# Kernel tuning notes

Hardware: AMD Instinct MI355X
Metric: run time of the kernel (lower is better)

## Reference

```python
import jax, jax.numpy as jnp
import numpy as np

B, L, NF, H = 4, 1024, 480, 32
FC = NF + H          # feat_i_classes = 512
D = FC               # downsample_feats (default None -> feat_i_classes)
W = 65               # positional window width (odd -> 'same' padding matches)
MAX0, MAX1 = 10.0, 100.0  # max_std_sigma_0 / max_std_sigma_1


def _uni(k, shape, lo=-0.01, hi=0.01):
    return jax.random.uniform(k, shape, jnp.float32, lo, hi)


def setup_inputs() -> dict:
    key = jax.random.key(0)
    ks = jax.random.split(key, 11)
    return {
        "x_embeds": jax.random.normal(ks[0], (B, L, NF), jnp.float32),
        "latent_outputs": jax.random.normal(ks[1], (B, L, H), jnp.float32),
        "masks": jnp.ones((B, L, 1), jnp.float32),
        "pos_embed": (jnp.arange(W, dtype=jnp.float32) - W // 2).reshape(W, 1, 1),
        "x": jax.random.uniform(ks[2], (B, L, 23), jnp.float32),
        "all_x_all_ampl": _uni(ks[3], (5, D, H)),
        "inp_decomp_vecs": _uni(ks[4], (5, D, 1)),
        "out_decomp_vecs": _uni(ks[5], (5, 1, H)),
        "all_x_all_bias": _uni(ks[6], (5, 1, H)),
        "pos_dep_ampl_weights": _uni(ks[7], (1, FC, H)),
        "knn_activations": _uni(ks[8], (2, FC, D)),
    }


def _conv_same(x_bdl, w_hdw):
    # torch F.conv1d (cross-correlation), stride 1, padding 'same'
    return jax.lax.conv_general_dilated(
        x_bdl, w_hdw, window_strides=(1,), padding="SAME",
        dimension_numbers=("NCH", "OIH", "NCH"))


def reference(x_embeds, latent_outputs, masks, pos_embed, x,
              all_x_all_ampl, inp_decomp_vecs, out_decomp_vecs,
              all_x_all_bias, pos_dep_ampl_weights, knn_activations):
    A = all_x_all_ampl                       # (5,D,H)
    rec = lambda i: inp_decomp_vecs[i] * out_decomp_vecs[i]  # (D,1)*(1,H)->(D,H)
    inv_c0 = 1.0 / MAX0 ** 2

    cls = jax.nn.softmax(latent_outputs * masks, axis=-1) * masks
    oef = jnp.concatenate([x_embeds, cls], axis=-1)          # (B,L,FC)
    cf0 = oef @ knn_activations[0]                           # (B,L,D)
    cf1 = oef @ knn_activations[1]                           # (B,L,D)

    def kern(ampl, mean, inv_var):
        # cos(0*pos+0)=1; pos (W,1,1) broadcast vs (D,H) -> (W,D,H)
        return jnp.exp(-inv_var * (pos_embed - mean) ** 2) * ampl

    # torch: std=abs(w)**0.5; inv_var = std**2 + 1/max0**2 = abs(w)+c
    k0 = kern(A[0], rec(0), jnp.abs(rec(1)) + inv_c0)
    k1 = kern(A[1], 0.0,    jnp.abs(rec(2)) + inv_c0)
    k2 = kern(A[2], rec(3), jnp.abs(rec(4)) + inv_c0)

    conv = lambda f, k: _conv_same(f.transpose(0, 2, 1),
                                   k.transpose(2, 1, 0)).transpose(0, 2, 1)
    acts0 = conv(cf0, k0)                                    # (B,L,H)
    acts1 = conv(cf1, k1)
    acts2 = conv(cf0, k2)

    b0, b1, b2, b3, class_mult = all_x_all_bias              # each (1,H)
    rec_dist_filt = (acts0 + b0) * acts1 \
        + acts2 * (cf1 @ A[1] + b2) \
        + (cf0 @ A[3] + b1) * (cf1 @ A[4])

    collect = jnp.sum(x[..., 21:], axis=-1, keepdims=True)   # (B,L,1)
    m = (masks + collect)[..., 0]                            # (B,L)
    pos = jnp.arange(L, dtype=jnp.float32)
    rel2 = (pos[None, :] - pos[:, None]) ** 2                # (L,L)
    sig = class_mult[0] ** 2 + 1.0 / MAX1 ** 2               # (H,)
    G = jnp.exp(-sig[:, None, None] * rel2)                  # (H,L,L)
    # V_correction[b,i,h] = m[b,i] * sum_j G[h,i,j] m[b,j]  (mask is rank-1)
    Vc = m[:, :, None] * jnp.einsum("hij,bj->bih", G, m)     # (B,L,H)

    per_pos = oef @ pos_dep_ampl_weights[0] + b3             # (B,L,H)
    return Vc * per_pos * rec_dist_filt * masks
```

## Files before the change

kernel.cpp:

```cpp
#include <hip/hip_runtime.h>
#include <hip/hip_bf16.h>

#define BB 4
#define LL 1024
#define NFE 480
#define HH 32
#define FCC 512
#define DD 512
#define WW 65
#define BL (BB*LL)
#define BLH (BL*HH)
#define LPAD 1088

typedef short bf16x8 __attribute__((ext_vector_type(8)));
typedef float f32x16 __attribute__((ext_vector_type(16)));
typedef unsigned short us8 __attribute__((ext_vector_type(8)));

__device__ inline unsigned short f2bf(float x) {
    union { float f; unsigned u; } v; v.f = x;
    unsigned r = v.u + 0x7FFFu + ((v.u >> 16) & 1u);
    return (unsigned short)(r >> 16);
}

__device__ __align__(16) unsigned short g_oefb[BL*FCC];
__device__ __align__(16) unsigned short g_knt[2*DD*FCC];
__device__ float  g_m[BL];
__device__ __align__(16) unsigned short g_fpad[2*BB*LPAD*DD];
__device__ __align__(16) unsigned short g_kb2[(size_t)3*WW*4*8*64*8];
__device__ __align__(16) unsigned short g_kbs[4*4*8*64*8];
__device__ float  g_actsp[4][3*BLH];
__device__ float  g_small[4*BLH];
__device__ float  g_gt[HH*LL];
__device__ float  g_vsum4[4][BLH];

__global__ __launch_bounds__(256) void kprep(const float* __restrict__ x_embeds,
                                             const float* __restrict__ latent,
                                             const float* __restrict__ masks,
                                             const float* __restrict__ x,
                                             const float* __restrict__ ampl,
                                             const float* __restrict__ inp,
                                             const float* __restrict__ outv,
                                             const float* __restrict__ pos,
                                             const float* __restrict__ bias,
                                             const float* __restrict__ pdw,
                                             const float* __restrict__ knn) {
    const int bx = blockIdx.x;
    const int tid = threadIdx.x;

    if (bx < 512) {
        const int row0 = bx * 8;
        const int r    = row0 + (tid >> 5);
        const int lane = tid & 31;

        const float mask = masks[r];
        float v = latent[r*HH + lane] * mask;
        float mx = v;
        #pragma unroll
        for (int off = 16; off > 0; off >>= 1) mx = fmaxf(mx, __shfl_xor(mx, off, 32));
        float e = __expf(v - mx);
        float s = e;
        #pragma unroll
        for (int off = 16; off > 0; off >>= 1) s += __shfl_xor(s, off, 32);
        g_oefb[r*FCC + NFE + lane] = f2bf(e / s * mask);

        if (lane == 0) g_m[r] = mask + x[r*23 + 21] + x[r*23 + 22];

        for (int idx = tid; idx < 8*NFE; idx += 256) {
            int rr = idx / NFE, c = idx - rr*NFE;
            g_oefb[(row0+rr)*FCC + c] = f2bf(x_embeds[(row0+rr)*NFE + c]);
        }
    } else if (bx < 640) {
        int idx = (bx - 512) * 256 + tid;
        int fzb = idx >> 12;
        int rem = idx & 4095;
        int rowi = rem >> 6;
        int col8 = rem & 63;
        int row = (rowi < 32) ? rowi : (1024 + rowi);
        int4 z = make_int4(0,0,0,0);
        *reinterpret_cast<int4*>(&g_fpad[((size_t)fzb*LPAD + row)*DD + col8*8]) = z;
    } else if (bx < 768) {
        __shared__ unsigned short tile[64][65];
        int idx2 = bx - 640;
        const int k0 = (idx2 & 7) * 64;
        const int n0 = ((idx2 >> 3) & 7) * 64;
        const int z  = idx2 >> 6;
        const float* __restrict__ src = knn + (size_t)z*FCC*DD;
        #pragma unroll 4
        for (int i = 0; i < 16; ++i) {
            int idx = i*256 + tid;
            int kk = idx >> 6, nn = idx & 63;
            tile[kk][nn] = f2bf(src[(size_t)(k0+kk)*DD + n0+nn]);
        }
        __syncthreads();
        #pragma unroll 4
        for (int i = 0; i < 16; ++i) {
            int idx = i*256 + tid;
            int nn = idx >> 6, kk = idx & 63;
            g_knt[((size_t)z*DD + n0+nn)*FCC + k0+kk] = tile[kk][nn];
        }
    } else if (bx < 800) {
        int t = (bx - 768)*256 + tid;
        int lane = t & 63;
        int ks = (t >> 6) & 7;
        int dt = (t >> 9) & 3;
        int o  = t >> 11;
        int l31 = lane & 31, khalf = lane >> 5;
        const float* S = (o == 0) ? ampl + 1*DD*HH :
                         (o == 1) ? ampl + 3*DD*HH :
                         (o == 2) ? ampl + 4*DD*HH : pdw;
        int k0 = dt*128 + ks*16 + khalf*8;
        us8 outw;
        #pragma unroll
        for (int i = 0; i < 8; ++i) outw[i] = f2bf(S[(size_t)(k0+i)*HH + l31]);
        *reinterpret_cast<us8*>(&g_kbs[(size_t)t*8]) = outw;
    } else if (bx < 928) {
        int idx = (bx - 800) * 256 + tid;
        int h = idx & 31;
        int dist = idx >> 5;
        float cm = bias[4*HH + h];
        float sig = cm*cm + 1e-4f;
        float dd = (float)dist;
        g_gt[idx] = __expf(-sig * dd * dd);
    } else {
        int idx3 = bx - 928;
        int xi  = idx3 & 7;
        int rem = idx3 >> 3;
        int w   = rem % 65;
        int z   = rem / 65;
        int idx = xi * 256 + tid;
        const int lane = idx & 63;
        const int ks   = (idx >> 6) & 7;
        const int dt   = idx >> 9;
        const int h    = lane & 31;
        const int d8   = dt*128 + ks*16 + (lane >> 5)*8;

        const float c0 = 0.01f;
        const float p = pos[w];
        int ai, mi, vi;
        if (z == 0)      { ai = 0; mi = 0;  vi = 1; }
        else if (z == 1) { ai = 1; mi = -1; vi = 2; }
        else             { ai = 2; mi = 3;  vi = 4; }

        us8 outw;
        #pragma unroll
        for (int i = 0; i < 8; ++i) {
            int d = d8 + i;
            float a    = ampl[(size_t)ai*DD*HH + d*HH + h];
            float mean = (mi >= 0) ? inp[mi*DD + d] * outv[mi*HH + h] : 0.f;
            float iv   = fabsf(inp[vi*DD + d] * outv[vi*HH + h]) + c0;
            float tt = p - mean;
            outw[i] = f2bf(__expf(-iv * tt * tt) * a);
        }
        *reinterpret_cast<us8*>(&g_kb2[((((size_t)z*WW + w)*4 + dt)*8 + ks)*512 + (size_t)lane*8]) = outw;
    }
}

__global__ __launch_bounds__(256) void k2_mfma() {
    const int nt = blockIdx.x;
    const int mt = blockIdx.y;
    const int z  = blockIdx.z;
    const int t  = threadIdx.x;
    const int wave = t >> 6, lane = t & 63;
    const int l31 = lane & 31, khalf = lane >> 5;
    const int n0 = nt*128 + wave*32;
    const int m_base = mt*64;

    __shared__ __align__(16) unsigned short smem[64*128];

    f32x16 acc[2];
    #pragma unroll
    for (int mti = 0; mti < 2; ++mti)
        #pragma unroll
        for (int i = 0; i < 16; ++i) acc[mti][i] = 0.f;

    const unsigned short* __restrict__ bptr =
        g_knt + ((size_t)z*DD + n0 + l31)*FCC + khalf*8;

    for (int kc = 0; kc < 4; ++kc) {
        __syncthreads();
        const unsigned short* __restrict__ src = g_oefb + (size_t)m_base*FCC + kc*128;
        #pragma unroll
        for (int c = 0; c < 4; ++c) {
            int q = c*256 + t;
            int row = q >> 4, slot = q & 15;
            int4 v = *reinterpret_cast<const int4*>(src + (size_t)row*FCC + slot*8);
            int off = row*256 + ((slot*16) ^ ((row & 15) << 4));
            *reinterpret_cast<int4*>((char*)smem + off) = v;
        }
        __syncthreads();
        #pragma unroll
        for (int ks = 0; ks < 8; ++ks) {
            bf16x8 bf = *reinterpret_cast<const bf16x8*>(bptr + kc*128 + ks*16);
            int dby = ks*32 + khalf*16;
            #pragma unroll
            for (int mti = 0; mti < 2; ++mti) {
                int r = mti*32 + l31;
                bf16x8 a = *reinterpret_cast<const bf16x8*>(
                    (char*)smem + r*256 + (dby ^ ((r & 15) << 4)));
                acc[mti] = __builtin_amdgcn_mfma_f32_32x32x16_bf16(a, bf, acc[mti], 0, 0, 0);
            }
        }
    }

    #pragma unroll
    for (int mti = 0; mti < 2; ++mti) {
        #pragma unroll
        for (int reg = 0; reg < 16; ++reg) {
            int rowf = (reg & 3) + 8*(reg >> 2) + 4*khalf;
            int m = m_base + mti*32 + rowf;
            int b_ = m >> 10, l_ = m & 1023;
            g_fpad[((size_t)(z*BB + b_)*LPAD + 32 + l_)*DD + n0 + l31] = f2bf(acc[mti][reg]);
        }
    }
}

__global__ __launch_bounds__(256) void kheavy() {
    __shared__ __align__(16) char smem_raw[32768];
    const int bx = blockIdx.x;
    const int t  = threadIdx.x;

    if (bx < 768) {
        const int xcd = bx & 7;
        const int j8  = bx >> 3;
        const int gidx = xcd*96 + j8;
        const int zdq = gidx >> 6;
        const int g   = gidx & 63;
        const int lt = g & 15;
        const int b  = g >> 4;
        const int z  = zdq >> 2;
        const int dq = zdq & 3;
        const int fz = (z == 1) ? 1 : 0;
        const int wave = t >> 6, lane = t & 63;
        const int l31 = lane & 31, khalf = lane >> 5;

        const int wbeg = (wave == 0) ? 0 : 17 + (wave - 1)*16;
        const int wend = (wave == 0) ? 17 : wbeg + 16;

        f32x16 acc0, acc1;
        #pragma unroll
        for (int i = 0; i < 16; ++i) { acc0[i] = 0.f; acc1[i] = 0.f; }

        const unsigned short* src =
            g_fpad + ((size_t)(fz*BB + b)*LPAD + lt*64) * DD + dq*128;
        #pragma unroll
        for (int c = 0; c < 8; ++c) {
            int q = c*256 + t;
            int row = q >> 4, slot = q & 15;
            int4 v = *reinterpret_cast<const int4*>(src + (size_t)row*DD + slot*8);
            int off = row*256 + ((slot*16) ^ ((row & 15) << 4));
            *reinterpret_cast<int4*>(smem_raw + off) = v;
        }
        __syncthreads();

        for (int w = wbeg; w < wend; ++w) {
            const unsigned short* kbw =
                g_kb2 + ((((size_t)z*WW + w)*4 + dq)*8)*512;
            const int r0 = l31 + w;
            const int r1 = r0 + 32;
            #pragma unroll
            for (int ks = 0; ks < 8; ++ks) {
                bf16x8 bf = *reinterpret_cast<const bf16x8*>(kbw + ks*512 + lane*8);
                int dby = ks*32 + khalf*16;
                bf16x8 a0 = *reinterpret_cast<const bf16x8*>(
                    smem_raw + r0*256 + (dby ^ ((r0 & 15) << 4)));
                bf16x8 a1 = *reinterpret_cast<const bf16x8*>(
                    smem_raw + r1*256 + (dby ^ ((r1 & 15) << 4)));
                acc0 = __builtin_amdgcn_mfma_f32_32x32x16_bf16(a0, bf, acc0, 0, 0, 0);
                acc1 = __builtin_amdgcn_mfma_f32_32x32x16_bf16(a1, bf, acc1, 0, 0, 0);
            }
        }

        __syncthreads();
        float* red = (float*)smem_raw;
        #pragma unroll
        for (int reg = 0; reg < 16; ++reg) {
            int row = (reg & 3) + 8*(reg >> 2) + 4*khalf;
            red[wave*2048 + row*32 + l31]        = acc0[reg];
            red[wave*2048 + (32 + row)*32 + l31] = acc1[reg];
        }
        __syncthreads();
        float* outp = g_actsp[dq] + (size_t)z*BLH + ((size_t)b*LL + lt*64)*HH;
        #pragma unroll
        for (int j = 0; j < 8; ++j) {
            int i = j*256 + t;
            float sum = red[i] + red[2048 + i] + red[4096 + i] + red[6144 + i];
            outp[i] = sum;
        }
    } else if (bx < 1280) {
        float* mlT = (float*)smem_raw;
        const int g  = bx - 768;
        const int jq = g >> 7;
        const int ib = g & 127;
        const int i0 = ib * 8;

        int wlo = i0 - 352; if (wlo < 0) wlo = 0; else wlo &= ~3;
        int whi = i0 + 360; if (whi > 1024) whi = 1024; else whi = (whi + 3) & ~3;
        int qstep = (((whi - wlo) + 15) >> 4) << 2;
        int qlo = wlo + jq*qstep;
        int qhi = qlo + qstep; if (qhi > whi) qhi = whi;
        int qn = qhi - qlo; if (qn < 0) qn = 0;

        for (int idx = t; idx < qn*4; idx += 256) {
            int jj = idx >> 2, b = idx & 3;
            mlT[jj*4 + b] = g_m[b*LL + qlo + jj];
        }
        __syncthreads();

        const int h = t & 31;
        const int i = i0 + (t >> 5);
        const float* __restrict__ gtt = g_gt;
        float a0 = 0.f, a1 = 0.f, a2 = 0.f, a3 = 0.f;
        #pragma unroll 2
        for (int jj = 0; jj < qn; ++jj) {
            int j = qlo + jj;
            int c = i - j; int d = c < 0 ? -c : c;
            float gv = gtt[d*HH + h];
            float4 mv = *reinterpret_cast<const float4*>(&mlT[jj*4]);
            a0 = fmaf(gv, mv.x, a0);
            a1 = fmaf(gv, mv.y, a1);
            a2 = fmaf(gv, mv.z, a2);
            a3 = fmaf(gv, mv.w, a3);
        }
        float* vs = g_vsum4[jq];
        vs[(size_t)(0*LL + i)*HH + h]      = a0;
        vs[(size_t)(1*LL + i)*HH + h + BLH/4*0 + 1*LL*HH*0] = a1;
        vs[((size_t)(1*LL + i))*HH + h] = a1;
        vs[((size_t)(2*LL + i))*HH + h] = a2;
        vs[((size_t)(3*LL + i))*HH + h] = a3;
    } else {
        const int g = bx - 1280;
        const int mt = g & 31;
        const int o  = g >> 5;
        const int wave = t >> 6, lane = t & 63;
        const int l31 = lane & 31, khalf = lane >> 5;

        const unsigned short* src;
        if (o == 3) {
            src = g_oefb + (size_t)mt*128*FCC;
        } else {
            const int fz = (o == 1) ? 0 : 1;
            const int m0 = mt*128;
            const int b_ = m0 >> 10, l0 = m0 & 1023;
            src = g_fpad + ((size_t)(fz*BB + b_)*LPAD + 32 + l0)*DD;
        }

        f32x16 acc;
        #pragma unroll
        for (int i = 0; i < 16; ++i) acc[i] = 0.f;

        for (int kc = 0; kc < 4; ++kc) {
            __syncthreads();
            const unsigned short* s2 = src + kc*128;
            #pragma unroll
            for (int c = 0; c < 8; ++c) {
                int q = c*256 + t;
                int row = q >> 4, slot = q & 15;
                int4 v = *reinterpret_cast<const int4*>(s2 + (size_t)row*512 + slot*8);
                int off = row*256 + ((slot*16) ^ ((row & 15) << 4));
                *reinterpret_cast<int4*>(smem_raw + off) = v;
            }
            __syncthreads();
            #pragma unroll
            for (int ks = 0; ks < 8; ++ks) {
                bf16x8 bf = *reinterpret_cast<const bf16x8*>(
                    &g_kbs[((((size_t)o*4 + kc)*8 + ks)*64 + lane)*8]);
                int dby = ks*32 + khalf*16;
                int r = wave*32 + l31;
                bf16x8 a = *reinterpret_cast<const bf16x8*>(
                    smem_raw + r*256 + (dby ^ ((r & 15) << 4)));
                acc = __builtin_amdgcn_mfma_f32_32x32x16_bf16(a, bf, acc, 0, 0, 0);
            }
        }

        float* outp = g_small + (size_t)o*BLH + ((size_t)mt*128 + wave*32)*HH;
        #pragma unroll
        for (int reg = 0; reg < 16; ++reg) {
            int row = (reg & 3) + 8*(reg >> 2) + 4*khalf;
            outp[(size_t)row*HH + l31] = acc[reg];
        }
    }
}

__global__ __launch_bounds__(256) void k7_final(const float* __restrict__ masks,
                                                const float* __restrict__ bias,
                                                float* __restrict__ out) {
    int idx = blockIdx.x * 256 + threadIdx.x;
    int r = idx >> 5, h = idx & 31;
    float a0 = 0.f, a1 = 0.f, a2 = 0.f;
    #pragma unroll
    for (int s = 0; s < 4; ++s) {
        a0 += g_actsp[s][idx];
        a1 += g_actsp[s][BLH + idx];
        a2 += g_actsp[s][2*BLH + idx];
    }
    float rdf = (a0 + bias[0*HH + h]) * a1
              + a2 * (g_small[idx] + bias[2*HH + h])
              + (g_small[BLH + idx] + bias[1*HH + h]) * g_small[2*BLH + idx];
    float pp = g_small[3*BLH + idx] + bias[3*HH + h];
    float vc = g_m[r] * (g_vsum4[0][idx] + g_vsum4[1][idx] + g_vsum4[2][idx] + g_vsum4[3][idx]);
    out[idx] = vc * pp * rdf * masks[r];
}

extern "C" void kernel_launch(void* const* d_in, const int* in_sizes, int n_in,
                              void* d_out, int out_size, void* d_ws, size_t ws_size,
                              hipStream_t stream) {
    (void)in_sizes; (void)n_in; (void)d_ws; (void)ws_size; (void)out_size;
    const float* x_embeds = (const float*)d_in[0];
    const float* latent   = (const float*)d_in[1];
    const float* masks    = (const float*)d_in[2];
    const float* pos      = (const float*)d_in[3];
    const float* x        = (const float*)d_in[4];
    const float* ampl     = (const float*)d_in[5];
    const float* inp      = (const float*)d_in[6];
    const float* outv     = (const float*)d_in[7];
    const float* bias     = (const float*)d_in[8];
    const float* pdw      = (const float*)d_in[9];
    const float* knn      = (const float*)d_in[10];
    float* out = (float*)d_out;

    hipLaunchKernelGGL(kprep, dim3(2488), dim3(256), 0, stream,
                       x_embeds, latent, masks, x, ampl, inp, outv, pos, bias, pdw, knn);
    hipLaunchKernelGGL(k2_mfma, dim3(4, 64, 2), dim3(256), 0, stream);
    hipLaunchKernelGGL(kheavy, dim3(1408), dim3(256), 0, stream);
    hipLaunchKernelGGL(k7_final, dim3(BLH/256), dim3(256), 0, stream, masks, bias, out);
}
```

Baseline: 77.53 us.

## Move Gaussian vsum into GEMM kernel and split conv window across twice the blocks

```diff
diff --git a/kernel.cpp b/kernel.cpp
--- a/kernel.cpp
+++ b/kernel.cpp
@@ -28,7 +28,7 @@
 __device__ __align__(16) unsigned short g_fpad[2*BB*LPAD*DD];
 __device__ __align__(16) unsigned short g_kb2[(size_t)3*WW*4*8*64*8];
 __device__ __align__(16) unsigned short g_kbs[4*4*8*64*8];
-__device__ float  g_actsp[4][3*BLH];
+__device__ float  g_actsp[8][3*BLH];
 __device__ float  g_small[4*BLH];
 __device__ float  g_gt[HH*LL];
 __device__ float  g_vsum4[4][BLH];
@@ -155,140 +155,69 @@
     }
 }
 
-__global__ __launch_bounds__(256) void k2_mfma() {
-    const int nt = blockIdx.x;
-    const int mt = blockIdx.y;
-    const int z  = blockIdx.z;
-    const int t  = threadIdx.x;
-    const int wave = t >> 6, lane = t & 63;
-    const int l31 = lane & 31, khalf = lane >> 5;
-    const int n0 = nt*128 + wave*32;
-    const int m_base = mt*64;
-
-    __shared__ __align__(16) unsigned short smem[64*128];
-
-    f32x16 acc[2];
-    #pragma unroll
-    for (int mti = 0; mti < 2; ++mti)
-        #pragma unroll
-        for (int i = 0; i < 16; ++i) acc[mti][i] = 0.f;
-
-    const unsigned short* __restrict__ bptr =
-        g_knt + ((size_t)z*DD + n0 + l31)*FCC + khalf*8;
-
-    for (int kc = 0; kc < 4; ++kc) {
-        __syncthreads();
-        const unsigned short* __restrict__ src = g_oefb + (size_t)m_base*FCC + kc*128;
-        #pragma unroll
-        for (int c = 0; c < 4; ++c) {
-            int q = c*256 + t;
-            int row = q >> 4, slot = q & 15;
-            int4 v = *reinterpret_cast<const int4*>(src + (size_t)row*FCC + slot*8);
-            int off = row*256 + ((slot*16) ^ ((row & 15) << 4));
-            *reinterpret_cast<int4*>((char*)smem + off) = v;
-        }
-        __syncthreads();
-        #pragma unroll
-        for (int ks = 0; ks < 8; ++ks) {
-            bf16x8 bf = *reinterpret_cast<const bf16x8*>(bptr + kc*128 + ks*16);
-            int dby = ks*32 + khalf*16;
-            #pragma unroll
-            for (int mti = 0; mti < 2; ++mti) {
-                int r = mti*32 + l31;
-                bf16x8 a = *reinterpret_cast<const bf16x8*>(
-                    (char*)smem + r*256 + (dby ^ ((r & 15) << 4)));
-                acc[mti] = __builtin_amdgcn_mfma_f32_32x32x16_bf16(a, bf, acc[mti], 0, 0, 0);
-            }
-        }
-    }
-
-    #pragma unroll
-    for (int mti = 0; mti < 2; ++mti) {
-        #pragma unroll
-        for (int reg = 0; reg < 16; ++reg) {
-            int rowf = (reg & 3) + 8*(reg >> 2) + 4*khalf;
-            int m = m_base + mti*32 + rowf;
-            int b_ = m >> 10, l_ = m & 1023;
-            g_fpad[((size_t)(z*BB + b_)*LPAD + 32 + l_)*DD + n0 + l31] = f2bf(acc[mti][reg]);
-        }
-    }
-}
-
-__global__ __launch_bounds__(256) void kheavy() {
-    __shared__ __align__(16) char smem_raw[32768];
+__global__ __launch_bounds__(256) void k2k6() {
+    __shared__ __align__(16) char smem_raw[16384];
     const int bx = blockIdx.x;
     const int t  = threadIdx.x;
 
-    if (bx < 768) {
-        const int xcd = bx & 7;
-        const int j8  = bx >> 3;
-        const int gidx = xcd*96 + j8;
-        const int zdq = gidx >> 6;
-        const int g   = gidx & 63;
-        const int lt = g & 15;
-        const int b  = g >> 4;
-        const int z  = zdq >> 2;
-        const int dq = zdq & 3;
-        const int fz = (z == 1) ? 1 : 0;
+    if (bx < 512) {
+        const int nt = bx & 3;
+        const int mt = (bx >> 2) & 63;
+        const int z  = bx >> 8;
         const int wave = t >> 6, lane = t & 63;
         const int l31 = lane & 31, khalf = lane >> 5;
-
-        const int wbeg = (wave == 0) ? 0 : 17 + (wave - 1)*16;
-        const int wend = (wave == 0) ? 17 : wbeg + 16;
-
-        f32x16 acc0, acc1;
-        #pragma unroll
-        for (int i = 0; i < 16; ++i) { acc0[i] = 0.f; acc1[i] = 0.f; }
-
-        const unsigned short* src =
-            g_fpad + ((size_t)(fz*BB + b)*LPAD + lt*64) * DD + dq*128;
-        #pragma unroll
-        for (int c = 0; c < 8; ++c) {
-            int q = c*256 + t;
-            int row = q >> 4, slot = q & 15;
-            int4 v = *reinterpret_cast<const int4*>(src + (size_t)row*DD + slot*8);
-            int off = row*256 + ((slot*16) ^ ((row & 15) << 4));
-            *reinterpret_cast<int4*>(smem_raw + off) = v;
-        }
-        __syncthreads();
-
-        for (int w = wbeg; w < wend; ++w) {
-            const unsigned short* kbw =
-                g_kb2 + ((((size_t)z*WW + w)*4 + dq)*8)*512;
-            const int r0 = l31 + w;
-            const int r1 = r0 + 32;
+        const int n0 = nt*128 + wave*32;
+        const int m_base = mt*64;
+        unsigned short* smem = (unsigned short*)smem_raw;
+
+        f32x16 acc[2];
+        #pragma unroll
+        for (int mti = 0; mti < 2; ++mti)
+            #pragma unroll
+            for (int i = 0; i < 16; ++i) acc[mti][i] = 0.f;
+
+        const unsigned short* __restrict__ bptr =
+            g_knt + ((size_t)z*DD + n0 + l31)*FCC + khalf*8;
+
+        for (int kc = 0; kc < 4; ++kc) {
+            __syncthreads();
+            const unsigned short* __restrict__ src = g_oefb + (size_t)m_base*FCC + kc*128;
+            #pragma unroll
+            for (int c = 0; c < 4; ++c) {
+                int q = c*256 + t;
+                int row = q >> 4, slot = q & 15;
+                int4 v = *reinterpret_cast<const int4*>(src + (size_t)row*FCC + slot*8);
+                int off = row*256 + ((slot*16) ^ ((row & 15) << 4));
+                *reinterpret_cast<int4*>(smem_raw + off) = v;
+            }
+            __syncthreads();
             #pragma unroll
             for (int ks = 0; ks < 8; ++ks) {
-                bf16x8 bf = *reinterpret_cast<const bf16x8*>(kbw + ks*512 + lane*8);
+                bf16x8 bf = *reinterpret_cast<const bf16x8*>(bptr + kc*128 + ks*16);
                 int dby = ks*32 + khalf*16;
-                bf16x8 a0 = *reinterpret_cast<const bf16x8*>(
-                    smem_raw + r0*256 + (dby ^ ((r0 & 15) << 4)));
-                bf16x8 a1 = *reinterpret_cast<const bf16x8*>(
-                    smem_raw + r1*256 + (dby ^ ((r1 & 15) << 4)));
-                acc0 = __builtin_amdgcn_mfma_f32_32x32x16_bf16(a0, bf, acc0, 0, 0, 0);
-                acc1 = __builtin_amdgcn_mfma_f32_32x32x16_bf16(a1, bf, acc1, 0, 0, 0);
-            }
-        }
-
-        __syncthreads();
-        float* red = (float*)smem_raw;
-        #pragma unroll
-        for (int reg = 0; reg < 16; ++reg) {
-            int row = (reg & 3) + 8*(reg >> 2) + 4*khalf;
-            red[wave*2048 + row*32 + l31]        = acc0[reg];
-            red[wave*2048 + (32 + row)*32 + l31] = acc1[reg];
-        }
-        __syncthreads();
-        float* outp = g_actsp[dq] + (size_t)z*BLH + ((size_t)b*LL + lt*64)*HH;
-        #pragma unroll
-        for (int j = 0; j < 8; ++j) {
-            int i = j*256 + t;
-            float sum = red[i] + red[2048 + i] + red[4096 + i] + red[6144 + i];
-            outp[i] = sum;
-        }
-    } else if (bx < 1280) {
+                #pragma unroll
+                for (int mti = 0; mti < 2; ++mti) {
+                    int r = mti*32 + l31;
+                    bf16x8 a = *reinterpret_cast<const bf16x8*>(
+                        smem_raw + r*256 + (dby ^ ((r & 15) << 4)));
+                    acc[mti] = __builtin_amdgcn_mfma_f32_32x32x16_bf16(a, bf, acc[mti], 0, 0, 0);
+                }
+            }
+        }
+
+        #pragma unroll
+        for (int mti = 0; mti < 2; ++mti) {
+            #pragma unroll
+            for (int reg = 0; reg < 16; ++reg) {
+                int rowf = (reg & 3) + 8*(reg >> 2) + 4*khalf;
+                int m = m_base + mti*32 + rowf;
+                int b_ = m >> 10, l_ = m & 1023;
+                g_fpad[((size_t)(z*BB + b_)*LPAD + 32 + l_)*DD + n0 + l31] = f2bf(acc[mti][reg]);
+            }
+        }
+    } else {
         float* mlT = (float*)smem_raw;
-        const int g  = bx - 768;
+        const int g  = bx - 512;
         const int jq = g >> 7;
         const int ib = g & 127;
         const int i0 = ib * 8;
@@ -322,13 +251,97 @@
             a3 = fmaf(gv, mv.w, a3);
         }
         float* vs = g_vsum4[jq];
-        vs[(size_t)(0*LL + i)*HH + h]      = a0;
-        vs[(size_t)(1*LL + i)*HH + h + BLH/4*0 + 1*LL*HH*0] = a1;
+        vs[((size_t)(0*LL + i))*HH + h] = a0;
         vs[((size_t)(1*LL + i))*HH + h] = a1;
         vs[((size_t)(2*LL + i))*HH + h] = a2;
         vs[((size_t)(3*LL + i))*HH + h] = a3;
+    }
+}
+
+__global__ __launch_bounds__(256) void kheavy() {
+    __shared__ __align__(16) char smem_raw[24576];
+    const int bx = blockIdx.x;
+    const int t  = threadIdx.x;
+
+    if (bx < 1536) {
+        const int hh  = bx & 1;
+        const int rest = bx >> 1;
+        const int lt = rest & 15;
+        const int b  = (rest >> 4) & 3;
+        const int zdq = rest >> 6;
+        const int z  = zdq >> 2;
+        const int dq = zdq & 3;
+        const int fz = (z == 1) ? 1 : 0;
+        const int wave = t >> 6, lane = t & 63;
+        const int l31 = lane & 31, khalf = lane >> 5;
+
+        int wbeg, wend;
+        if (hh == 0) { wbeg = (wave == 0) ? 0 : 9 + (wave - 1)*8; wend = (wave == 0) ? 9 : wbeg + 8; }
+        else         { wbeg = 33 + wave*8; wend = wbeg + 8; }
+
+        f32x16 acc0, acc1;
+        #pragma unroll
+        for (int i = 0; i < 16; ++i) { acc0[i] = 0.f; acc1[i] = 0.f; }
+
+        const unsigned short* src =
+            g_fpad + ((size_t)(fz*BB + b)*LPAD + lt*64 + hh*32) * DD + dq*128;
+        #pragma unroll
+        for (int c = 0; c < 6; ++c) {
+            int q = c*256 + t;
+            int row = q >> 4, slot = q & 15;
+            int4 v = *reinterpret_cast<const int4*>(src + (size_t)row*DD + slot*8);
+            int off = row*256 + ((slot*16) ^ ((row & 15) << 4));
+            *reinterpret_cast<int4*>(smem_raw + off) = v;
+        }
+        __syncthreads();
+
+        const int rsub = hh*32;
+        for (int w = wbeg; w < wend; ++w) {
+            const unsigned short* kbw =
+                g_kb2 + ((((size_t)z*WW + w)*4 + dq)*8)*512;
+            const int rl0 = l31 + w - rsub;
+            const int rl1 = rl0 + 32;
+            #pragma unroll
+            for (int ks = 0; ks < 8; ++ks) {
+                bf16x8 bf = *reinterpret_cast<const bf16x8*>(kbw + ks*512 + lane*8);
+                int dby = ks*32 + khalf*16;
+                bf16x8 a0 = *reinterpret_cast<const bf16x8*>(
+                    smem_raw + rl0*256 + (dby ^ ((rl0 & 15) << 4)));
+                bf16x8 a1 = *reinterpret_cast<const bf16x8*>(
+                    smem_raw + rl1*256 + (dby ^ ((rl1 & 15) << 4)));
+                acc0 = __builtin_amdgcn_mfma_f32_32x32x16_bf16(a0, bf, acc0, 0, 0, 0);
+                acc1 = __builtin_amdgcn_mfma_f32_32x32x16_bf16(a1, bf, acc1, 0, 0, 0);
+            }
+        }
+
+        float* red = (float*)smem_raw;
+        float* outp = g_actsp[dq*2 + hh] + (size_t)z*BLH + ((size_t)b*LL + lt*64)*HH;
+        __syncthreads();
+        #pragma unroll
+        for (int reg = 0; reg < 16; ++reg) {
+            int row = (reg & 3) + 8*(reg >> 2) + 4*khalf;
+            red[wave*1024 + row*32 + l31] = acc0[reg];
+        }
+        __syncthreads();
+        #pragma unroll
+        for (int j = 0; j < 4; ++j) {
+            int i = j*256 + t;
+            outp[i] = red[i] + red[1024 + i] + red[2048 + i] + red[3072 + i];
+        }
+        __syncthreads();
+        #pragma unroll
+        for (int reg = 0; reg < 16; ++reg) {
+            int row = (reg & 3) + 8*(reg >> 2) + 4*khalf;
+            red[wave*1024 + row*32 + l31] = acc1[reg];
+        }
+        __syncthreads();
+        #pragma unroll
+        for (int j = 0; j < 4; ++j) {
+            int i = j*256 + t;
+            outp[32*HH + i] = red[i] + red[1024 + i] + red[2048 + i] + red[3072 + i];
+        }
     } else {
-        const int g = bx - 1280;
+        const int g = bx - 1536;
         const int mt = g & 31;
         const int o  = g >> 5;
         const int wave = t >> 6, lane = t & 63;
@@ -348,26 +361,29 @@
         #pragma unroll
         for (int i = 0; i < 16; ++i) acc[i] = 0.f;
 
-        for (int kc = 0; kc < 4; ++kc) {
+        for (int kc64 = 0; kc64 < 8; ++kc64) {
             __syncthreads();
-            const unsigned short* s2 = src + kc*128;
-            #pragma unroll
-            for (int c = 0; c < 8; ++c) {
+            const unsigned short* s2 = src + kc64*64;
+            #pragma unroll
+            for (int c = 0; c < 4; ++c) {
                 int q = c*256 + t;
-                int row = q >> 4, slot = q & 15;
+                int row = q >> 3, slot = q & 7;
                 int4 v = *reinterpret_cast<const int4*>(s2 + (size_t)row*512 + slot*8);
-                int off = row*256 + ((slot*16) ^ ((row & 15) << 4));
+                int off = row*128 + ((slot*16) ^ ((row & 7) << 4));
                 *reinterpret_cast<int4*>(smem_raw + off) = v;
             }
             __syncthreads();
-            #pragma unroll
-            for (int ks = 0; ks < 8; ++ks) {
+            const int kc = kc64 >> 1;
+            const int ksb = (kc64 & 1)*4;
+            #pragma unroll
+            for (int ksl = 0; ksl < 4; ++ksl) {
+                int ks = ksb + ksl;
                 bf16x8 bf = *reinterpret_cast<const bf16x8*>(
                     &g_kbs[((((size_t)o*4 + kc)*8 + ks)*64 + lane)*8]);
-                int dby = ks*32 + khalf*16;
+                int dby = ksl*32 + khalf*16;
                 int r = wave*32 + l31;
                 bf16x8 a = *reinterpret_cast<const bf16x8*>(
-                    smem_raw + r*256 + (dby ^ ((r & 15) << 4)));
+                    smem_raw + r*128 + (dby ^ ((r & 7) << 4)));
                 acc = __builtin_amdgcn_mfma_f32_32x32x16_bf16(a, bf, acc, 0, 0, 0);
             }
         }
@@ -388,7 +404,7 @@
     int r = idx >> 5, h = idx & 31;
     float a0 = 0.f, a1 = 0.f, a2 = 0.f;
     #pragma unroll
-    for (int s = 0; s < 4; ++s) {
+    for (int s = 0; s < 8; ++s) {
         a0 += g_actsp[s][idx];
         a1 += g_actsp[s][BLH + idx];
         a2 += g_actsp[s][2*BLH + idx];
@@ -420,7 +436,7 @@
 
     hipLaunchKernelGGL(kprep, dim3(2488), dim3(256), 0, stream,
                        x_embeds, latent, masks, x, ampl, inp, outv, pos, bias, pdw, knn);
-    hipLaunchKernelGGL(k2_mfma, dim3(4, 64, 2), dim3(256), 0, stream);
-    hipLaunchKernelGGL(kheavy, dim3(1408), dim3(256), 0, stream);
+    hipLaunchKernelGGL(k2k6, dim3(1024), dim3(256), 0, stream);
+    hipLaunchKernelGGL(kheavy, dim3(1664), dim3(256), 0, stream);
     hipLaunchKernelGGL(k7_final, dim3(BLH/256), dim3(256), 0, stream, masks, bias, out);
 }
```

Measured after the change: 80.61 us. 4.0% more time.

## Split conv waves by row half and window half, drop LDS reduction

Applied to the files above, without the earlier changes.

```diff
diff --git a/kernel.cpp b/kernel.cpp
--- a/kernel.cpp
+++ b/kernel.cpp
@@ -28,7 +28,7 @@
 __device__ __align__(16) unsigned short g_fpad[2*BB*LPAD*DD];
 __device__ __align__(16) unsigned short g_kb2[(size_t)3*WW*4*8*64*8];
 __device__ __align__(16) unsigned short g_kbs[4*4*8*64*8];
-__device__ float  g_actsp[4][3*BLH];
+__device__ float  g_actsp[8][3*BLH];
 __device__ float  g_small[4*BLH];
 __device__ float  g_gt[HH*LL];
 __device__ float  g_vsum4[4][BLH];
@@ -232,13 +232,14 @@
         const int fz = (z == 1) ? 1 : 0;
         const int wave = t >> 6, lane = t & 63;
         const int l31 = lane & 31, khalf = lane >> 5;
-
-        const int wbeg = (wave == 0) ? 0 : 17 + (wave - 1)*16;
-        const int wend = (wave == 0) ? 17 : wbeg + 16;
-
-        f32x16 acc0, acc1;
-        #pragma unroll
-        for (int i = 0; i < 16; ++i) { acc0[i] = 0.f; acc1[i] = 0.f; }
+        const int s  = wave & 1;
+        const int hh = wave >> 1;
+        const int wbeg = hh ? 33 : 0;
+        const int wend = hh ? 65 : 33;
+
+        f32x16 acc;
+        #pragma unroll
+        for (int i = 0; i < 16; ++i) acc[i] = 0.f;
 
         const unsigned short* src =
             g_fpad + ((size_t)(fz*BB + b)*LPAD + lt*64) * DD + dq*128;
@@ -255,36 +256,24 @@
         for (int w = wbeg; w < wend; ++w) {
             const unsigned short* kbw =
                 g_kb2 + ((((size_t)z*WW + w)*4 + dq)*8)*512;
-            const int r0 = l31 + w;
-            const int r1 = r0 + 32;
+            const int rl = s*32 + l31 + w;
+            const int rbase = rl*256;
+            const int rx = (rl & 15) << 4;
             #pragma unroll
             for (int ks = 0; ks < 8; ++ks) {
                 bf16x8 bf = *reinterpret_cast<const bf16x8*>(kbw + ks*512 + lane*8);
                 int dby = ks*32 + khalf*16;
-                bf16x8 a0 = *reinterpret_cast<const bf16x8*>(
-                    smem_raw + r0*256 + (dby ^ ((r0 & 15) << 4)));
-                bf16x8 a1 = *reinterpret_cast<const bf16x8*>(
-                    smem_raw + r1*256 + (dby ^ ((r1 & 15) << 4)));
-                acc0 = __builtin_amdgcn_mfma_f32_32x32x16_bf16(a0, bf, acc0, 0, 0, 0);
-                acc1 = __builtin_amdgcn_mfma_f32_32x32x16_bf16(a1, bf, acc1, 0, 0, 0);
+                bf16x8 a = *reinterpret_cast<const bf16x8*>(
+                    smem_raw + rbase + (dby ^ rx));
+                acc = __builtin_amdgcn_mfma_f32_32x32x16_bf16(a, bf, acc, 0, 0, 0);
             }
         }
 
-        __syncthreads();
-        float* red = (float*)smem_raw;
+        float* outp = g_actsp[dq*2 + hh] + (size_t)z*BLH + ((size_t)b*LL + lt*64)*HH;
         #pragma unroll
         for (int reg = 0; reg < 16; ++reg) {
-            int row = (reg & 3) + 8*(reg >> 2) + 4*khalf;
-            red[wave*2048 + row*32 + l31]        = acc0[reg];
-            red[wave*2048 + (32 + row)*32 + l31] = acc1[reg];
-        }
-        __syncthreads();
-        float* outp = g_actsp[dq] + (size_t)z*BLH + ((size_t)b*LL + lt*64)*HH;
-        #pragma unroll
-        for (int j = 0; j < 8; ++j) {
-            int i = j*256 + t;
-            float sum = red[i] + red[2048 + i] + red[4096 + i] + red[6144 + i];
-            outp[i] = sum;
+            int rowf = (reg & 3) + 8*(reg >> 2) + 4*khalf;
+            outp[(size_t)(s*32 + rowf)*HH + l31] = acc[reg];
         }
     } else if (bx < 1280) {
         float* mlT = (float*)smem_raw;
@@ -322,8 +311,7 @@
             a3 = fmaf(gv, mv.w, a3);
         }
         float* vs = g_vsum4[jq];
-        vs[(size_t)(0*LL + i)*HH + h]      = a0;
-        vs[(size_t)(1*LL + i)*HH + h + BLH/4*0 + 1*LL*HH*0] = a1;
+        vs[((size_t)(0*LL + i))*HH + h] = a0;
         vs[((size_t)(1*LL + i))*HH + h] = a1;
         vs[((size_t)(2*LL + i))*HH + h] = a2;
         vs[((size_t)(3*LL + i))*HH + h] = a3;
@@ -388,7 +376,7 @@
     int r = idx >> 5, h = idx & 31;
     float a0 = 0.f, a1 = 0.f, a2 = 0.f;
     #pragma unroll
-    for (int s = 0; s < 4; ++s) {
+    for (int s = 0; s < 8; ++s) {
         a0 += g_actsp[s][idx];
         a1 += g_actsp[s][BLH + idx];
         a2 += g_actsp[s][2*BLH + idx];
```

New measurement: 90.41 us. 1.17x slower.
